# Optimization experiments

Hardware: AMD Instinct MI355X
Metric: run time of the kernel (lower is better)

The kernel has to match this reference:

```python
import jax, jax.numpy as jnp
import numpy as np

NEG = -1e30  # log-space 'zero' that stays finite in fp32
EPS = 1e-7   # keras backend epsilon used by ctc_batch_cost


def _lse3(a, b, c):
    m = jnp.maximum(jnp.maximum(a, b), c)
    return m + jnp.log(jnp.exp(a - m) + jnp.exp(b - m) + jnp.exp(c - m))


def setup_inputs() -> dict:
    key = jax.random.key(0)
    k1, k2 = jax.random.split(key)
    B, T, C, U = 256, 1024, 128, 128
    logits = jax.random.normal(k1, (B, T, C), dtype=jnp.float32)
    y_pred = jax.nn.softmax(logits, axis=-1)  # ctc_batch_cost expects probabilities
    y_true = jax.random.randint(k2, (B, U), 0, C - 1)  # labels in [0, C-2]; blank = C-1
    return {"y_true": y_true, "y_pred": y_pred}


def reference(y_true, y_pred):
    # Faithful to tf.keras.backend.ctc_batch_cost with input_length = T,
    # label_length = U for every row; blank index = num_classes - 1.
    B, T, C = y_pred.shape
    U = y_true.shape[1]
    S = 2 * U + 1
    blank = C - 1

    logp = jnp.log(y_pred + EPS)  # [B, T, C]

    # Extended label sequence: blank, l1, blank, l2, ..., lU, blank
    ext = jnp.full((B, S), blank, dtype=y_true.dtype).at[:, 1::2].set(y_true)

    # Per-timestep log-probs of extended labels: [B, T, S]
    lp_ext = jnp.take_along_axis(logp, jnp.broadcast_to(ext[:, None, :], (B, T, S)), axis=2)

    # Skip transition s-2 -> s allowed iff ext[s] != blank and ext[s] != ext[s-2]
    allow = jnp.concatenate(
        [jnp.zeros((B, 2), bool), (ext[:, 2:] != blank) & (ext[:, 2:] != ext[:, :-2])],
        axis=1,
    )  # [B, S]

    alpha0 = (
        jnp.full((B, S), NEG, dtype=logp.dtype)
        .at[:, 0].set(lp_ext[:, 0, 0])
        .at[:, 1].set(lp_ext[:, 0, 1])
    )

    lp_t = jnp.moveaxis(lp_ext, 1, 0)  # [T, B, S]

    def step(alpha, lp):
        a1 = jnp.concatenate([jnp.full((B, 1), NEG, alpha.dtype), alpha[:, :-1]], axis=1)
        a2 = jnp.concatenate([jnp.full((B, 2), NEG, alpha.dtype), alpha[:, :-2]], axis=1)
        a2 = jnp.where(allow, a2, NEG)
        alpha = _lse3(alpha, a1, a2) + lp
        return alpha, None

    alphaT, _ = jax.lax.scan(step, alpha0, lp_t[1:])

    a, b = alphaT[:, S - 1], alphaT[:, S - 2]
    m = jnp.maximum(a, b)
    ll = m + jnp.log(jnp.exp(a - m) + jnp.exp(b - m))
    return (-ll)[:, None]  # [B, 1], matching ctc_batch_cost
```

## Files before the change

### kernel.cpp

```cpp
#include <hip/hip_runtime.h>
#include <math.h>


#define T_DIM 1024
#define C_DIM 128
#define U_DIM 128
#define LN2F  0.6931471805599453f


#define EPS_LIT "0x33d6bf95"

#define ROWLOAD(Q1,Q3,QB) \
  "global_load_dword " Q1 ", v20, %[P]\n\t" \
  "global_load_dword " Q3 ", v21, %[P]\n\t" \
  "global_load_dword " QB ", v22, %[P] offset:508\n\t" \
  "v_add_u32 v20, 0x200, v20\n\t" \
  "v_add_u32 v21, 0x200, v21\n\t" \
  "v_add_u32 v22, 0x200, v22\n\t"

#define COMMIT(Q1,Q3,QB) \
  "v_add_f32 v27, " EPS_LIT ", " Q1 "\n\t" \
  "v_add_f32 v28, " EPS_LIT ", " Q3 "\n\t" \
  "v_add_f32 v26, " EPS_LIT ", " QB "\n\t"

#define ALPHA \
  "v_mov_b32_dpp v23, %[A3] wave_shr:1 row_mask:0xf bank_mask:0xf bound_ctrl:0\n\t" \
  "v_add_f32 v24, %[A0], v23\n\t" \
  "v_add_f32 v25, %[A0], %[A1]\n\t" \
  "v_fma_f32 v25, v23, v30, v25\n\t" \
  "v_mul_f32 %[A0], v24, v26\n\t" \
  "v_add_f32 v24, %[A1], %[A2]\n\t" \
  "v_add_f32 v23, %[A2], %[A3]\n\t" \
  "v_fma_f32 v23, %[A1], v31, v23\n\t" \
  "v_mul_f32 %[A1], v25, v27\n\t" \
  "v_mul_f32 %[A2], v24, v26\n\t" \
  "v_add_f32 v24, %[A3], %[A4]\n\t" \
  "v_mul_f32 %[A3], v23, v28\n\t" \
  "v_mul_f32 %[A4], v24, v26\n\t"

#define RENORM \
  "v_max_f32 v29, %[A0], %[A1]\n\t" \
  "v_max_f32 v29, v29, %[A2]\n\t" \
  "v_max_f32 v29, v29, %[A3]\n\t" \
  "v_max_f32 v29, v29, %[A4]\n\t" \
  "s_nop 1\n\t" \
  "v_max_f32_dpp v29, v29, v29 row_ror:8 row_mask:0xf bank_mask:0xf\n\t" \
  "s_nop 1\n\t" \
  "v_max_f32_dpp v29, v29, v29 row_ror:4 row_mask:0xf bank_mask:0xf\n\t" \
  "s_nop 1\n\t" \
  "v_max_f32_dpp v29, v29, v29 row_ror:2 row_mask:0xf bank_mask:0xf\n\t" \
  "s_nop 1\n\t" \
  "v_max_f32_dpp v29, v29, v29 row_ror:1 row_mask:0xf bank_mask:0xf\n\t" \
  "s_nop 1\n\t" \
  "v_readlane_b32 s91, v29, 0\n\t" \
  "v_readlane_b32 s92, v29, 16\n\t" \
  "v_readlane_b32 s93, v29, 32\n\t" \
  "v_readlane_b32 s94, v29, 48\n\t" \
  "s_nop 1\n\t" \
  "s_max_u32 s91, s91, s92\n\t" \
  "s_max_u32 s93, s93, s94\n\t" \
  "s_max_u32 s91, s91, s93\n\t" \
  "s_lshr_b32 s92, s91, 23\n\t" \
  "s_and_b32 s92, s92, 0xff\n\t" \
  "s_sub_u32 s93, 0x126, s92\n\t" \
  "s_min_u32 s93, s93, 0xfe\n\t" \
  "s_lshl_b32 s94, s93, 23\n\t" \
  "s_sub_u32 s95, 0x7f, s93\n\t" \
  "s_add_u32 %[EA], %[EA], s95\n\t" \
  "v_mul_f32 %[A0], s94, %[A0]\n\t" \
  "v_mul_f32 %[A1], s94, %[A1]\n\t" \
  "v_mul_f32 %[A2], s94, %[A2]\n\t" \
  "v_mul_f32 %[A3], s94, %[A3]\n\t" \
  "v_mul_f32 %[A4], s94, %[A4]\n\t"

#define STEP(Q1,Q3,QB) \
  "s_waitcnt vmcnt(45)\n\t" COMMIT(Q1,Q3,QB) ROWLOAD(Q1,Q3,QB) ALPHA
#define STEPR(Q1,Q3,QB)  STEP(Q1,Q3,QB) RENORM
#define ESTEP(Q1,Q3,QB)  COMMIT(Q1,Q3,QB) ALPHA
#define ESTEPR(Q1,Q3,QB) ESTEP(Q1,Q3,QB) RENORM

__global__ __launch_bounds__(64) void ctc_alpha_kernel(
    const int*   __restrict__ y_true,
    const float* __restrict__ y_pred,
    float*       __restrict__ out,
    int B)
{
  const int b = blockIdx.x;
  if (b >= B) return;
  const int lane = threadIdx.x;
  const float* __restrict__ p  = y_pred + (size_t)b * (T_DIM * C_DIM);
  const int*   __restrict__ yb = y_true + b * U_DIM;
  const int blank = C_DIM - 1;

  const int ylab0 = yb[2 * lane];
  const int ylab1 = yb[2 * lane + 1];
  int yprev = blank;
  if (lane > 0) yprev = yb[2 * lane - 1];
  const float allow1 = (lane > 0 && ylab0 != blank && ylab0 != yprev) ? 1.0f : 0.0f;
  const float allow3 = (ylab1 != blank && ylab1 != ylab0)             ? 1.0f : 0.0f;

  const int o1 = ylab0 * 4;
  const int o3 = ylab1 * 4;

  float a0 = (lane == 0) ? 1.0f : 0.0f;
  float a1 = 0.f, a2 = 0.f, a3 = 0.f, a4 = 0.f;
  int   e_acc = 0;

  asm volatile(
    "v_mov_b32 v20, %[O1]\n\t"
    "v_mov_b32 v21, %[O3]\n\t"
    "v_mov_b32 v22, 0\n\t"
    "v_mov_b32 v30, %[L1]\n\t"
    "v_mov_b32 v31, %[L3]\n\t"
    ROWLOAD("v32","v48","v64") ROWLOAD("v33","v49","v65")
    ROWLOAD("v34","v50","v66") ROWLOAD("v35","v51","v67")
    ROWLOAD("v36","v52","v68") ROWLOAD("v37","v53","v69")
    ROWLOAD("v38","v54","v70") ROWLOAD("v39","v55","v71")
    ROWLOAD("v40","v56","v72") ROWLOAD("v41","v57","v73")
    ROWLOAD("v42","v58","v74") ROWLOAD("v43","v59","v75")
    ROWLOAD("v44","v60","v76") ROWLOAD("v45","v61","v77")
    ROWLOAD("v46","v62","v78") ROWLOAD("v47","v63","v79")
    "s_mov_b32 s90, 63\n"
    "Lmain_%=:\n\t"
    STEP ("v32","v48","v64")
    STEP ("v33","v49","v65")
    STEP ("v34","v50","v66")
    STEP ("v35","v51","v67")
    STEP ("v36","v52","v68")
    STEP ("v37","v53","v69")
    STEP ("v38","v54","v70")
    STEPR("v39","v55","v71")
    STEP ("v40","v56","v72")
    STEP ("v41","v57","v73")
    STEP ("v42","v58","v74")
    STEP ("v43","v59","v75")
    STEP ("v44","v60","v76")
    STEP ("v45","v61","v77")
    STEP ("v46","v62","v78")
    STEPR("v47","v63","v79")
    "s_sub_u32 s90, s90, 1\n\t"
    "s_cmp_lg_u32 s90, 0\n\t"
    "s_cbranch_scc1 Lmain_%=\n\t"
    "s_waitcnt vmcnt(0)\n\t"
    ESTEP ("v32","v48","v64")
    ESTEP ("v33","v49","v65")
    ESTEP ("v34","v50","v66")
    ESTEP ("v35","v51","v67")
    ESTEP ("v36","v52","v68")
    ESTEP ("v37","v53","v69")
    ESTEP ("v38","v54","v70")
    ESTEPR("v39","v55","v71")
    ESTEP ("v40","v56","v72")
    ESTEP ("v41","v57","v73")
    ESTEP ("v42","v58","v74")
    ESTEP ("v43","v59","v75")
    ESTEP ("v44","v60","v76")
    ESTEP ("v45","v61","v77")
    ESTEP ("v46","v62","v78")
    ESTEP ("v47","v63","v79")
    : [A0]"+v"(a0), [A1]"+v"(a1), [A2]"+v"(a2), [A3]"+v"(a3), [A4]"+v"(a4),
      [EA]"+s"(e_acc)
    : [P]"s"(p), [O1]"v"(o1), [O3]"v"(o3), [L1]"v"(allow1), [L3]"v"(allow3)
    : "v20","v21","v22","v23","v24","v25","v26","v27","v28","v29","v30","v31",
      "v32","v33","v34","v35","v36","v37","v38","v39","v40","v41","v42","v43",
      "v44","v45","v46","v47","v48","v49","v50","v51","v52","v53","v54","v55",
      "v56","v57","v58","v59","v60","v61","v62","v63","v64","v65","v66","v67",
      "v68","v69","v70","v71","v72","v73","v74","v75","v76","v77","v78","v79",
      "s90","s91","s92","s93","s94","s95","scc","memory");

  if (lane == 63) {
    float s = a3 + a4;
    s = fmaxf(s, 1e-37f);
    float ll = logf(s) + (float)e_acc * LN2F;
    out[b] = -ll;
  }
}

extern "C" void kernel_launch(void* const* d_in, const int* in_sizes, int n_in,
                              void* d_out, int out_size, void* d_ws, size_t ws_size,
                              hipStream_t stream) {
  const int*   y_true = (const int*)d_in[0];
  const float* y_pred = (const float*)d_in[1];
  float*       out    = (float*)d_out;
  const int B = in_sizes[0] / U_DIM;
  ctc_alpha_kernel<<<dim3(B), dim3(64), 0, stream>>>(y_true, y_pred, out, B);
}
```

Measured before the change: 202.4 us.

## Stage probability rows through LDS with coalesced dwordx4 loads instead of gathers

Each step's data path changes: the kernel no longer issues three per-lane global gathers per timestep. It now loads two full class rows per iteration with a coalesced global_load_dwordx4, writes them to a 16KB LDS ring, and reads the two label probabilities plus the blank probability back with ds_read. This targets the cost of scattered 4-byte global gathers and the high vmcnt pressure. The trade is extra LDS write and read latency on the serial alpha recurrence and tighter lgkmcnt ordering, which the hand-written waitcnt schedule must get right.

New measurement: 200.5 us. Within noise of the previous version (-0.9%).

```diff
diff --git a/kernel.cpp b/kernel.cpp
--- a/kernel.cpp
+++ b/kernel.cpp
@@ -7,21 +7,18 @@
 #define U_DIM 128
 #define LN2F  0.6931471805599453f
 
-
 #define EPS_LIT "0x33d6bf95"
 
-#define ROWLOAD(Q1,Q3,QB) \
-  "global_load_dword " Q1 ", v20, %[P]\n\t" \
-  "global_load_dword " Q3 ", v21, %[P]\n\t" \
-  "global_load_dword " QB ", v22, %[P] offset:508\n\t" \
-  "v_add_u32 v20, 0x200, v20\n\t" \
-  "v_add_u32 v21, 0x200, v21\n\t" \
-  "v_add_u32 v22, 0x200, v22\n\t"
-
-#define COMMIT(Q1,Q3,QB) \
-  "v_add_f32 v27, " EPS_LIT ", " Q1 "\n\t" \
-  "v_add_f32 v28, " EPS_LIT ", " Q3 "\n\t" \
-  "v_add_f32 v26, " EPS_LIT ", " QB "\n\t"
+
+#define RD(RC1,RC3,RCB,ROFF,RBOFF) \
+  "ds_read_b32 " RC1 ", v12 offset:" ROFF "\n\t" \
+  "ds_read_b32 " RC3 ", v13 offset:" ROFF "\n\t" \
+  "ds_read_b32 " RCB ", v14 offset:" RBOFF "\n\t"
+
+#define CMT(RC1,RC3,RCB) \
+  "v_add_f32 v27, " EPS_LIT ", " RC1 "\n\t" \
+  "v_add_f32 v28, " EPS_LIT ", " RC3 "\n\t" \
+  "v_add_f32 v26, " EPS_LIT ", " RCB "\n\t"
 
 #define ALPHA \
   "v_mov_b32_dpp v23, %[A3] wave_shr:1 row_mask:0xf bank_mask:0xf bound_ctrl:0\n\t" \
@@ -73,11 +70,29 @@
   "v_mul_f32 %[A3], s94, %[A3]\n\t" \
   "v_mul_f32 %[A4], s94, %[A4]\n\t"
 
-#define STEP(Q1,Q3,QB) \
-  "s_waitcnt vmcnt(45)\n\t" COMMIT(Q1,Q3,QB) ROWLOAD(Q1,Q3,QB) ALPHA
-#define STEPR(Q1,Q3,QB)  STEP(Q1,Q3,QB) RENORM
-#define ESTEP(Q1,Q3,QB)  COMMIT(Q1,Q3,QB) ALPHA
-#define ESTEPR(Q1,Q3,QB) ESTEP(Q1,Q3,QB) RENORM
+#define SE(QW,WOFF,QL,RBOFF) \
+  "s_waitcnt vmcnt(14)\n\t" \
+  "ds_write_b128 v11, v[" QW "] offset:" WOFF "\n\t" \
+  "global_load_dwordx4 v[" QL "], v10, %[P]\n\t" \
+  "v_add_u32 v10, 0x400, v10\n\t" \
+  "s_waitcnt lgkmcnt(4)\n\t" \
+  CMT("v16","v17","v18") \
+  RD("v16","v17","v18", WOFF, RBOFF) \
+  ALPHA
+
+#define SO(ROFF,RBOFF) \
+  "s_waitcnt lgkmcnt(4)\n\t" \
+  CMT("v19","v20","v21") \
+  RD("v19","v20","v21", ROFF, RBOFF) \
+  ALPHA
+
+#define TE(VC,QW,WOFF,RBOFF) \
+  "s_waitcnt vmcnt(" VC ")\n\t" \
+  "ds_write_b128 v11, v[" QW "] offset:" WOFF "\n\t" \
+  "s_waitcnt lgkmcnt(4)\n\t" \
+  CMT("v16","v17","v18") \
+  RD("v16","v17","v18", WOFF, RBOFF) \
+  ALPHA
 
 __global__ __launch_bounds__(64) void ctc_alpha_kernel(
     const int*   __restrict__ y_true,
@@ -85,6 +100,8 @@
     float*       __restrict__ out,
     int B)
 {
+  __shared__ float4 ldsbuf[1024];
+
   const int b = blockIdx.x;
   if (b >= B) return;
   const int lane = threadIdx.x;
@@ -99,73 +116,101 @@
   const float allow1 = (lane > 0 && ylab0 != blank && ylab0 != yprev) ? 1.0f : 0.0f;
   const float allow3 = (ylab1 != blank && ylab1 != ylab0)             ? 1.0f : 0.0f;
 
-  const int o1 = ylab0 * 4;
-  const int o3 = ylab1 * 4;
+  const unsigned lds_off = (unsigned)(uintptr_t)(void*)ldsbuf;
+  const int gvoff = lane * 16;
+  const int wraddr = (int)lds_off + lane * 16;
+  const int rd1    = (int)lds_off + ylab0 * 4;
+  const int rd3    = (int)lds_off + ylab1 * 4;
+  const int rdb    = (int)lds_off;
 
   float a0 = (lane == 0) ? 1.0f : 0.0f;
   float a1 = 0.f, a2 = 0.f, a3 = 0.f, a4 = 0.f;
   int   e_acc = 0;
 
   asm volatile(
-    "v_mov_b32 v20, %[O1]\n\t"
-    "v_mov_b32 v21, %[O3]\n\t"
-    "v_mov_b32 v22, 0\n\t"
+    "s_mov_b32 m0, -1\n\t"
+    "v_mov_b32 v10, %[GV]\n\t"
+    "v_mov_b32 v11, %[WA]\n\t"
+    "v_mov_b32 v12, %[R1]\n\t"
+    "v_mov_b32 v13, %[R3]\n\t"
+    "v_mov_b32 v14, %[RB]\n\t"
     "v_mov_b32 v30, %[L1]\n\t"
     "v_mov_b32 v31, %[L3]\n\t"
-    ROWLOAD("v32","v48","v64") ROWLOAD("v33","v49","v65")
-    ROWLOAD("v34","v50","v66") ROWLOAD("v35","v51","v67")
-    ROWLOAD("v36","v52","v68") ROWLOAD("v37","v53","v69")
-    ROWLOAD("v38","v54","v70") ROWLOAD("v39","v55","v71")
-    ROWLOAD("v40","v56","v72") ROWLOAD("v41","v57","v73")
-    ROWLOAD("v42","v58","v74") ROWLOAD("v43","v59","v75")
-    ROWLOAD("v44","v60","v76") ROWLOAD("v45","v61","v77")
-    ROWLOAD("v46","v62","v78") ROWLOAD("v47","v63","v79")
-    "s_mov_b32 s90, 63\n"
-    "Lmain_%=:\n\t"
-    STEP ("v32","v48","v64")
-    STEP ("v33","v49","v65")
-    STEP ("v34","v50","v66")
-    STEP ("v35","v51","v67")
-    STEP ("v36","v52","v68")
-    STEP ("v37","v53","v69")
-    STEP ("v38","v54","v70")
-    STEPR("v39","v55","v71")
-    STEP ("v40","v56","v72")
-    STEP ("v41","v57","v73")
-    STEP ("v42","v58","v74")
-    STEP ("v43","v59","v75")
-    STEP ("v44","v60","v76")
-    STEP ("v45","v61","v77")
-    STEP ("v46","v62","v78")
-    STEPR("v47","v63","v79")
+    "global_load_dwordx4 v[32:35], v10, %[P]\n\t" "v_add_u32 v10, 0x400, v10\n\t"
+    "global_load_dwordx4 v[36:39], v10, %[P]\n\t" "v_add_u32 v10, 0x400, v10\n\t"
+    "global_load_dwordx4 v[40:43], v10, %[P]\n\t" "v_add_u32 v10, 0x400, v10\n\t"
+    "global_load_dwordx4 v[44:47], v10, %[P]\n\t" "v_add_u32 v10, 0x400, v10\n\t"
+    "global_load_dwordx4 v[48:51], v10, %[P]\n\t" "v_add_u32 v10, 0x400, v10\n\t"
+    "global_load_dwordx4 v[52:55], v10, %[P]\n\t" "v_add_u32 v10, 0x400, v10\n\t"
+    "global_load_dwordx4 v[56:59], v10, %[P]\n\t" "v_add_u32 v10, 0x400, v10\n\t"
+    "global_load_dwordx4 v[60:63], v10, %[P]\n\t" "v_add_u32 v10, 0x400, v10\n\t"
+    "global_load_dwordx4 v[64:67], v10, %[P]\n\t" "v_add_u32 v10, 0x400, v10\n\t"
+    "global_load_dwordx4 v[68:71], v10, %[P]\n\t" "v_add_u32 v10, 0x400, v10\n\t"
+    "global_load_dwordx4 v[72:75], v10, %[P]\n\t" "v_add_u32 v10, 0x400, v10\n\t"
+    "global_load_dwordx4 v[76:79], v10, %[P]\n\t" "v_add_u32 v10, 0x400, v10\n\t"
+    "global_load_dwordx4 v[80:83], v10, %[P]\n\t" "v_add_u32 v10, 0x400, v10\n\t"
+    "global_load_dwordx4 v[84:87], v10, %[P]\n\t" "v_add_u32 v10, 0x400, v10\n\t"
+    "global_load_dwordx4 v[88:91], v10, %[P]\n\t" "v_add_u32 v10, 0x400, v10\n\t"
+    "global_load_dwordx4 v[92:95], v10, %[P]\n\t" "v_add_u32 v10, 0x400, v10\n\t"
+    "s_waitcnt vmcnt(15)\n\t"
+    "ds_write_b128 v11, v[32:35] offset:0\n\t"
+    RD("v16","v17","v18", "0",   "508")
+    RD("v19","v20","v21", "512", "1020")
+    "s_mov_b32 s90, 31\n"
+    "LM_%=:\n\t"
+    SE("36:39","1024","32:35","1532")   SO("1536","2044")
+    SE("40:43","2048","36:39","2556")   SO("2560","3068")
+    SE("44:47","3072","40:43","3580")   SO("3584","4092")
+    SE("48:51","4096","44:47","4604")   SO("4608","5116")   RENORM
+    SE("52:55","5120","48:51","5628")   SO("5632","6140")
+    SE("56:59","6144","52:55","6652")   SO("6656","7164")
+    SE("60:63","7168","56:59","7676")   SO("7680","8188")
+    SE("64:67","8192","60:63","8700")   SO("8704","9212")   RENORM
+    SE("68:71","9216","64:67","9724")   SO("9728","10236")
+    SE("72:75","10240","68:71","10748") SO("10752","11260")
+    SE("76:79","11264","72:75","11772") SO("11776","12284")
+    SE("80:83","12288","76:79","12796") SO("12800","13308") RENORM
+    SE("84:87","13312","80:83","13820") SO("13824","14332")
+    SE("88:91","14336","84:87","14844") SO("14848","15356")
+    SE("92:95","15360","88:91","15868") SO("15872","16380")
+    SE("32:35","0","92:95","508")       SO("512","1020")    RENORM
     "s_sub_u32 s90, s90, 1\n\t"
     "s_cmp_lg_u32 s90, 0\n\t"
-    "s_cbranch_scc1 Lmain_%=\n\t"
-    "s_waitcnt vmcnt(0)\n\t"
-    ESTEP ("v32","v48","v64")
-    ESTEP ("v33","v49","v65")
-    ESTEP ("v34","v50","v66")
-    ESTEP ("v35","v51","v67")
-    ESTEP ("v36","v52","v68")
-    ESTEP ("v37","v53","v69")
-    ESTEP ("v38","v54","v70")
-    ESTEPR("v39","v55","v71")
-    ESTEP ("v40","v56","v72")
-    ESTEP ("v41","v57","v73")
-    ESTEP ("v42","v58","v74")
-    ESTEP ("v43","v59","v75")
-    ESTEP ("v44","v60","v76")
-    ESTEP ("v45","v61","v77")
-    ESTEP ("v46","v62","v78")
-    ESTEP ("v47","v63","v79")
+    "s_cbranch_scc1 LM_%=\n\t"
+    TE("14","36:39","1024","1532")   SO("1536","2044")
+    TE("13","40:43","2048","2556")   SO("2560","3068")
+    TE("12","44:47","3072","3580")   SO("3584","4092")
+    TE("11","48:51","4096","4604")   SO("4608","5116")   RENORM
+    TE("10","52:55","5120","5628")   SO("5632","6140")
+    TE("9","56:59","6144","6652")    SO("6656","7164")
+    TE("8","60:63","7168","7676")    SO("7680","8188")
+    TE("7","64:67","8192","8700")    SO("8704","9212")   RENORM
+    TE("6","68:71","9216","9724")    SO("9728","10236")
+    TE("5","72:75","10240","10748")  SO("10752","11260")
+    TE("4","76:79","11264","11772")  SO("11776","12284")
+    TE("3","80:83","12288","12796")  SO("12800","13308") RENORM
+    TE("2","84:87","13312","13820")  SO("13824","14332")
+    TE("1","88:91","14336","14844")  SO("14848","15356")
+    TE("0","92:95","15360","15868")  SO("15872","16380")
+    "s_waitcnt lgkmcnt(3)\n\t"
+    CMT("v16","v17","v18")
+    ALPHA
+    "s_waitcnt lgkmcnt(0)\n\t"
+    CMT("v19","v20","v21")
+    ALPHA
+    RENORM
     : [A0]"+v"(a0), [A1]"+v"(a1), [A2]"+v"(a2), [A3]"+v"(a3), [A4]"+v"(a4),
       [EA]"+s"(e_acc)
-    : [P]"s"(p), [O1]"v"(o1), [O3]"v"(o3), [L1]"v"(allow1), [L3]"v"(allow3)
-    : "v20","v21","v22","v23","v24","v25","v26","v27","v28","v29","v30","v31",
+    : [P]"s"(p), [GV]"v"(gvoff), [WA]"v"(wraddr), [R1]"v"(rd1), [R3]"v"(rd3),
+      [RB]"v"(rdb), [L1]"v"(allow1), [L3]"v"(allow3)
+    : "v10","v11","v12","v13","v14","v15","v16","v17","v18","v19","v20","v21",
+      "v22","v23","v24","v25","v26","v27","v28","v29","v30","v31",
       "v32","v33","v34","v35","v36","v37","v38","v39","v40","v41","v42","v43",
       "v44","v45","v46","v47","v48","v49","v50","v51","v52","v53","v54","v55",
       "v56","v57","v58","v59","v60","v61","v62","v63","v64","v65","v66","v67",
       "v68","v69","v70","v71","v72","v73","v74","v75","v76","v77","v78","v79",
+      "v80","v81","v82","v83","v84","v85","v86","v87","v88","v89","v90","v91",
+      "v92","v93","v94","v95",
       "s90","s91","s92","s93","s94","s95","scc","memory");
 
   if (lane == 63) {
```
